# Optimization experiments

Hardware: AMD Instinct MI355X
Metric: run time of the kernel (lower is better)

The kernel has to match this reference:

```python
import jax, jax.numpy as jnp
import numpy as np

EPS = 1e-5
N_HEADS = 16
D_NOPE = 128
D_ROPE = 64
D_QK = D_NOPE + D_ROPE  # 192
D_V = 128
KV_RANK = 512
SCALE = D_QK ** -0.5


def rms_norm(x, w, eps=EPS):
    return x * jax.lax.rsqrt(jnp.mean(x * x, axis=-1, keepdims=True) + eps) * w


def apply_rope(x, c, s):
    # x: [..., D_ROPE], c/s broadcastable [..., D_ROPE//2]; half-split rotation
    x0, x1 = x[..., : D_ROPE // 2], x[..., D_ROPE // 2 :]
    return jnp.concatenate([x0 * c - x1 * s, x0 * s + x1 * c], axis=-1)


def setup_inputs() -> dict:
    key = jax.random.key(0)
    ks = jax.random.split(key, 8)
    B, S, H_DIM = 2, 2048, 2048
    Q_RANK = 1536
    w = lambda k, shp: jax.random.normal(k, shp, dtype=jnp.float32) * 0.02
    # real RoPE tables: [max_seq, D_ROPE//2]
    inv_freq = 1.0 / (10000.0 ** (np.arange(0, D_ROPE, 2, dtype=np.float32) / D_ROPE))
    ang = np.arange(S, dtype=np.float32)[:, None] * inv_freq[None, :]
    return {
        "x": jax.random.normal(ks[0], (B, S, H_DIM), dtype=jnp.float32),
        "positions": jnp.arange(S, dtype=jnp.int64),
        "Wqa": w(ks[1], (H_DIM, Q_RANK)),
        "g_qa": jnp.ones((Q_RANK,), jnp.float32),
        "Wqb": w(ks[2], (Q_RANK, N_HEADS * D_QK)),
        "Wkva": w(ks[3], (H_DIM, KV_RANK + D_ROPE)),
        "g_kva": jnp.ones((KV_RANK,), jnp.float32),
        "Wkvb": w(ks[4], (KV_RANK, N_HEADS * (D_NOPE + D_V))),
        "Wo": w(ks[5], (N_HEADS * D_V, H_DIM)),
        "cos": jnp.asarray(np.cos(ang)),
        "sin": jnp.asarray(np.sin(ang)),
    }


def reference(x, positions, Wqa, g_qa, Wqb, Wkva, g_kva, Wkvb, Wo, cos, sin):
    B, S, _ = x.shape
    # Q path: low-rank down, RMSNorm, up
    q = rms_norm(x @ Wqa, g_qa) @ Wqb  # [B,S,H*D_QK]
    q = q.reshape(B, S, N_HEADS, D_QK)
    q_nope, q_rope = q[..., :D_NOPE], q[..., D_NOPE:]
    c = cos[positions]  # [S, D_ROPE//2]
    s = sin[positions]
    q_rope = apply_rope(q_rope, c[None, :, None, :], s[None, :, None, :])
    # KV path: joint down-proj, split latent / rope-key
    kv_a = x @ Wkva  # [B,S,KV_RANK+D_ROPE]
    kv_latent = rms_norm(kv_a[..., :KV_RANK], g_kva)
    k_rope = apply_rope(kv_a[..., KV_RANK:], c[None, :, :], s[None, :, :])  # [B,S,D_ROPE]
    # up-project latent to per-head k_nope and v
    kv_b = (kv_latent @ Wkvb).reshape(B, S, N_HEADS, D_NOPE + D_V)
    k_nope, v = kv_b[..., :D_NOPE], kv_b[..., D_NOPE:]
    k = jnp.concatenate(
        [k_nope, jnp.broadcast_to(k_rope[:, :, None, :], (B, S, N_HEADS, D_ROPE))], axis=-1
    )  # [B,S,H,D_QK]
    q_full = jnp.concatenate([q_nope, q_rope], axis=-1)  # [B,S,H,D_QK]
    # causal SDPA with d_qk != d_v
    scores = jnp.einsum("bqhd,bkhd->bhqk", q_full, k) * SCALE
    causal = jnp.tril(jnp.ones((S, S), dtype=bool))
    scores = jnp.where(causal[None, None, :, :], scores, -jnp.inf)
    p = jax.nn.softmax(scores, axis=-1)
    out = jnp.einsum("bhqk,bkhd->bqhd", p, v).reshape(B, S, N_HEADS * D_V)
    return out @ Wo
```

## Files before the change

kernel.cpp:

```cpp
#include <hip/hip_runtime.h>
#include <hip/hip_bf16.h>

typedef __bf16 bf16;
typedef __bf16 bf16x8 __attribute__((ext_vector_type(8)));
typedef __bf16 bf16x4 __attribute__((ext_vector_type(4)));
typedef float f32x4 __attribute__((ext_vector_type(4)));

#define B_    2
#define S_    2048
#define HD    2048
#define NH    16
#define DQK   192
#define DV    128
#define QR    1536
#define KVR   512
#define NTOK  4096
#define NKVB  4096
#define NQB   3072
#define NQKVA 2176

static __device__ __forceinline__ void gload16(const void* g, void* l) {
  __builtin_amdgcn_global_load_lds(
      (const __attribute__((address_space(1))) void*)g,
      (__attribute__((address_space(3))) void*)l, 16, 0, 0);
}

__global__ __launch_bounds__(256) void cvt_bf16(const float* __restrict__ in,
                                                bf16* __restrict__ out, long n) {
  long i = ((long)blockIdx.x * 256 + threadIdx.x) * 4;
  if (i + 3 < n) {
    float4 v = *(const float4*)(in + i);
    bf16x4 o = {(bf16)v.x, (bf16)v.y, (bf16)v.z, (bf16)v.w};
    *(bf16x4*)(out + i) = o;
  }
}

__global__ __launch_bounds__(256) void transpose_cvt(const float* __restrict__ in,
                                                     bf16* __restrict__ out,
                                                     int R, int C, int Np) {
  __shared__ float tile[32][33];
  int c0 = blockIdx.x * 32;
  int r0 = blockIdx.y * 32;
  int tx = threadIdx.x & 31, ty = threadIdx.x >> 5;
#pragma unroll
  for (int i = 0; i < 4; ++i) {
    int r = r0 + ty + i * 8, c = c0 + tx;
    tile[ty + i * 8][tx] = (c < C) ? in[(long)r * C + c] : 0.f;
  }
  __syncthreads();
#pragma unroll
  for (int i = 0; i < 4; ++i) {
    int oc = c0 + ty + i * 8;
    if (oc < Np) out[(long)oc * R + r0 + tx] = (bf16)tile[tx][ty + i * 8];
  }
}

#define GEMM_CORE(A, Bt, K)                                                    \
  __shared__ bf16 As[128 * 64];                                                \
  __shared__ bf16 Bs[128 * 64];                                                \
  const int t = threadIdx.x;                                                   \
  const int l = t & 63;                                                        \
  const int w = t >> 6;                                                        \
  const int m0 = blockIdx.y * 128;                                             \
  const int n0 = blockIdx.x * 128;                                             \
  const int wr = (w >> 1) * 64;                                                \
  const int wc = (w & 1) * 64;                                                 \
  const int lr = l & 15;                                                       \
  const int lg = l >> 4;                                                       \
  f32x4 acc[4][4] = {};                                                        \
  for (int k0 = 0; k0 < (K); k0 += 64) {                                       \
    __syncthreads();                                                           \
    _Pragma("unroll")                                                          \
    for (int j = 0; j < 4; ++j) {                                              \
      int s = j * 256 + t;                                                     \
      int row = s >> 3, sc = s & 7;                                            \
      int c = sc ^ (row & 7);                                                  \
      gload16((A) + (long)(m0 + row) * (K) + k0 + c * 8,                       \
              As + (j * 256 + w * 64) * 8);                                    \
      gload16((Bt) + (long)(n0 + row) * (K) + k0 + c * 8,                      \
              Bs + (j * 256 + w * 64) * 8);                                    \
    }                                                                          \
    __syncthreads();                                                           \
    _Pragma("unroll")                                                          \
    for (int kh = 0; kh < 2; ++kh) {                                           \
      bf16x8 af[4], bfr[4];                                                    \
      _Pragma("unroll")                                                        \
      for (int m = 0; m < 4; ++m) {                                            \
        int row = wr + m * 16 + lr;                                            \
        af[m] = *(const bf16x8*)(As + row * 64 + (((kh * 4 + lg) ^ (row & 7)) << 3)); \
      }                                                                        \
      _Pragma("unroll")                                                        \
      for (int n = 0; n < 4; ++n) {                                            \
        int row = wc + n * 16 + lr;                                            \
        bfr[n] = *(const bf16x8*)(Bs + row * 64 + (((kh * 4 + lg) ^ (row & 7)) << 3)); \
      }                                                                        \
      _Pragma("unroll")                                                        \
      for (int m = 0; m < 4; ++m)                                              \
        _Pragma("unroll")                                                      \
        for (int n = 0; n < 4; ++n)                                            \
          acc[m][n] = __builtin_amdgcn_mfma_f32_16x16x32_bf16(af[m], bfr[n], acc[m][n], 0, 0, 0); \
    }                                                                          \
  }

template <typename CT>
__global__ __launch_bounds__(256) void gemm_bf16(const bf16* __restrict__ A,
                                                 const bf16* __restrict__ Bt,
                                                 CT* __restrict__ C,
                                                 int M, int N, int K) {
  GEMM_CORE(A, Bt, K)
#pragma unroll
  for (int m = 0; m < 4; ++m)
#pragma unroll
    for (int n = 0; n < 4; ++n)
#pragma unroll
      for (int v = 0; v < 4; ++v) {
        int row = m0 + wr + m * 16 + lg * 4 + v;
        int col = n0 + wc + n * 16 + lr;
        C[(long)row * N + col] = (CT)acc[m][n][v];
      }
}

__global__ __launch_bounds__(256) void gemm_qf(const bf16* __restrict__ A,
                                               const bf16* __restrict__ Bt,
                                               const int* __restrict__ pos,
                                               const float* __restrict__ cosT,
                                               const float* __restrict__ sinT,
                                               bf16* __restrict__ q_bhsd) {
  const float SCALE = 0.07216878364870323f;
  GEMM_CORE(A, Bt, QR)
  int c0 = n0 + wc;
  int h = c0 / 192;
  int part = c0 - h * 192;
#pragma unroll
  for (int m = 0; m < 4; ++m)
#pragma unroll
    for (int v = 0; v < 4; ++v) {
      int row = m0 + wr + m * 16 + lg * 4 + v;
      int b = row >> 11, s = row & (S_ - 1);
      long base = ((long)(b * NH + h) * S_ + s) * DQK;
      if (part < 128) {
#pragma unroll
        for (int n = 0; n < 4; ++n)
          q_bhsd[base + part + n * 16 + lr] = (bf16)(acc[m][n][v] * SCALE);
      } else {
        int p = pos[s] & (S_ - 1);
        float c_lo = cosT[p * 32 + lr],      s_lo = sinT[p * 32 + lr];
        float c_hi = cosT[p * 32 + 16 + lr], s_hi = sinT[p * 32 + 16 + lr];
        float o0 = acc[m][0][v] * c_lo - acc[m][2][v] * s_lo;
        float o1 = acc[m][1][v] * c_hi - acc[m][3][v] * s_hi;
        float o2 = acc[m][0][v] * s_lo + acc[m][2][v] * c_lo;
        float o3 = acc[m][1][v] * s_hi + acc[m][3][v] * c_hi;
        q_bhsd[base + 128 + lr] = (bf16)(o0 * SCALE);
        q_bhsd[base + 144 + lr] = (bf16)(o1 * SCALE);
        q_bhsd[base + 160 + lr] = (bf16)(o2 * SCALE);
        q_bhsd[base + 176 + lr] = (bf16)(o3 * SCALE);
      }
    }
}

__global__ __launch_bounds__(256) void gemm_kvb(const bf16* __restrict__ A,
                                                const bf16* __restrict__ Bt,
                                                bf16* __restrict__ k_bhsd,
                                                bf16* __restrict__ v_rows) {
  GEMM_CORE(A, Bt, KVR)
  int c0 = n0 + wc;
  int h = c0 >> 8;
  int dbase = c0 & 64;
  bool vpart = (c0 >> 7) & 1;
#pragma unroll
  for (int m = 0; m < 4; ++m)
#pragma unroll
    for (int v = 0; v < 4; ++v) {
      int row = m0 + wr + m * 16 + lg * 4 + v;
      int b = row >> 11, s = row & (S_ - 1);
      if (!vpart) {
        long base = ((long)(b * NH + h) * S_ + s) * DQK + dbase;
#pragma unroll
        for (int n = 0; n < 4; ++n)
          k_bhsd[base + n * 16 + lr] = (bf16)acc[m][n][v];
      } else {
        long base = (long)row * 2048 + h * 128 + dbase;
#pragma unroll
        for (int n = 0; n < 4; ++n)
          v_rows[base + n * 16 + lr] = (bf16)acc[m][n][v];
      }
    }
}

__global__ __launch_bounds__(192) void rmsnorm_q(const bf16* __restrict__ in,
                                                 const float* __restrict__ g,
                                                 bf16* __restrict__ out) {
  int row = blockIdx.x;
  int t = threadIdx.x;
  const bf16* x = in + (long)row * NQKVA;
  bf16x8 vv = *(const bf16x8*)(x + t * 8);
  float vf[8]; float ss = 0.f;
#pragma unroll
  for (int e = 0; e < 8; ++e) { vf[e] = (float)vv[e]; ss += vf[e] * vf[e]; }
#pragma unroll
  for (int m = 1; m < 64; m <<= 1) ss += __shfl_xor(ss, m);
  __shared__ float red[3];
  if ((t & 63) == 0) red[t >> 6] = ss;
  __syncthreads();
  ss = red[0] + red[1] + red[2];
  float rs = rsqrtf(ss / QR + 1e-5f);
  bf16x8 o;
#pragma unroll
  for (int e = 0; e < 8; ++e) o[e] = (bf16)(vf[e] * rs * g[t * 8 + e]);
  *(bf16x8*)(out + (long)row * QR + t * 8) = o;
}

__global__ __launch_bounds__(64) void kv_prep(const bf16* __restrict__ xa,
                                              const float* __restrict__ g,
                                              const int* __restrict__ pos,
                                              const float* __restrict__ cosT,
                                              const float* __restrict__ sinT,
                                              bf16* __restrict__ kv_l,
                                              bf16* __restrict__ k_bhsd) {
  int row = blockIdx.x;
  int t = threadIdx.x;
  int b = row >> 11, s = row & (S_ - 1);
  const bf16* x = xa + (long)row * NQKVA + QR;
  bf16x8 vv = *(const bf16x8*)(x + t * 8);
  float vf[8]; float ss = 0.f;
#pragma unroll
  for (int e = 0; e < 8; ++e) { vf[e] = (float)vv[e]; ss += vf[e] * vf[e]; }
#pragma unroll
  for (int m = 1; m < 64; m <<= 1) ss += __shfl_xor(ss, m);
  float rs = rsqrtf(ss / KVR + 1e-5f);
  bf16x8 o;
#pragma unroll
  for (int e = 0; e < 8; ++e) o[e] = (bf16)(vf[e] * rs * g[t * 8 + e]);
  *(bf16x8*)(kv_l + (long)row * KVR + t * 8) = o;
  __shared__ bf16 rope_s[64];
  if (t < 32) {
    int p = pos[s] & (S_ - 1);
    float c = cosT[p * 32 + t], sn = sinT[p * 32 + t];
    float x0 = (float)x[512 + t], x1 = (float)x[544 + t];
    rope_s[t] = (bf16)(x0 * c - x1 * sn);
    rope_s[32 + t] = (bf16)(x0 * sn + x1 * c);
  }
  __syncthreads();
  bf16x8 rv = *(const bf16x8*)&rope_s[(t & 7) * 8];
  long base0 = ((long)(b * NH + (t >> 3)) * S_ + s) * DQK + 128 + (t & 7) * 8;
  long base1 = ((long)(b * NH + 8 + (t >> 3)) * S_ + s) * DQK + 128 + (t & 7) * 8;
  *(bf16x8*)(k_bhsd + base0) = rv;
  *(bf16x8*)(k_bhsd + base1) = rv;
}

__global__ __launch_bounds__(256) void v_trans(const bf16* __restrict__ v_rows,
                                               bf16* __restrict__ v_t) {
  __shared__ bf16 tile[32][33];
  int st = blockIdx.x, dt = blockIdx.y, bh = blockIdx.z;
  int b = bh >> 4, h = bh & 15;
  int tx = threadIdx.x & 31, ty = threadIdx.x >> 5;
#pragma unroll
  for (int i = 0; i < 4; ++i) {
    int s = st * 32 + ty + i * 8, d = dt * 32 + tx;
    tile[ty + i * 8][tx] = v_rows[((long)(b * S_ + s)) * 2048 + h * 128 + d];
  }
  __syncthreads();
#pragma unroll
  for (int i = 0; i < 4; ++i) {
    int d = dt * 32 + ty + i * 8, s = st * 32 + tx;
    v_t[((long)bh * DV + d) * S_ + s] = tile[tx][ty + i * 8];
  }
}

#define QBLK 64
#define KVB  64
__global__ __launch_bounds__(256) void flash2(const bf16* __restrict__ q_bhsd,
                                              const bf16* __restrict__ k_bhsd,
                                              const bf16* __restrict__ v_t,
                                              bf16* __restrict__ att) {
  __shared__ bf16 Ks[KVB * DQK];
  __shared__ bf16 Vs[DV * KVB];
  __shared__ bf16 Ps[4][16 * 72];
  int bid = blockIdx.x;
  int bh = bid & 31;
  int qt = 31 - (bid >> 5);
  int b = bh >> 4, h = bh & 15;
  int q0 = qt * QBLK;
  int t = threadIdx.x;
  int w = t >> 6, l = t & 63;
  int lr = l & 15, lg = l >> 4;
  int qw = q0 + w * 16;

  const bf16* Qb = q_bhsd + (long)bh * S_ * DQK;
  const bf16* Kb = k_bhsd + (long)bh * S_ * DQK;
  const bf16* Vb = v_t + (long)bh * DV * S_;

  bf16x8 qf[6];
#pragma unroll
  for (int t6 = 0; t6 < 6; ++t6)
    qf[t6] = *(const bf16x8*)(Qb + (long)(qw + lr) * DQK + t6 * 32 + lg * 8);

  f32x4 oacc[8] = {};
  float mrow[4] = {-1e30f, -1e30f, -1e30f, -1e30f};
  float lrow[4] = {0.f, 0.f, 0.f, 0.f};
  const int lr7 = lr & 7;

  int nkt = qt + 1;
  for (int kt = 0; kt < nkt; ++kt) {
    int k0 = kt * KVB;
    __syncthreads();
#pragma unroll
    for (int j = 0; j < 6; ++j) {
      int s = j * 256 + t;
      int r = s / 24, c1 = s - r * 24;
      int c = c1 ^ (r & 7);
      gload16(Kb + (long)(k0 + r) * DQK + c * 8, Ks + (j * 256 + w * 64) * 8);
    }
#pragma unroll
    for (int j = 0; j < 4; ++j) {
      int s = j * 256 + t;
      int d = s >> 3, c1 = s & 7;
      int c = c1 ^ (d & 7);
      gload16(Vb + (long)d * S_ + k0 + c * 8, Vs + (j * 256 + w * 64) * 8);
    }
    __syncthreads();
    if (k0 > qw + 15) continue;

    f32x4 sacc[4] = {};
#pragma unroll
    for (int n = 0; n < 4; ++n) {
      int rk = n * 16 + lr;
#pragma unroll
      for (int t6 = 0; t6 < 6; ++t6) {
        bf16x8 kf = *(const bf16x8*)(Ks + rk * DQK + (((t6 * 4 + lg) ^ lr7) << 3));
        sacc[n] = __builtin_amdgcn_mfma_f32_16x16x32_bf16(qf[t6], kf, sacc[n], 0, 0, 0);
      }
    }
    if (k0 + KVB - 1 > qw) {
#pragma unroll
      for (int n = 0; n < 4; ++n)
#pragma unroll
        for (int v = 0; v < 4; ++v) {
          int r = lg * 4 + v, c = n * 16 + lr;
          if (k0 + c > qw + r) sacc[n][v] = -1e30f;
        }
    }
    float corr[4], p[4][4];
#pragma unroll
    for (int v = 0; v < 4; ++v) {
      float mv = fmaxf(fmaxf(sacc[0][v], sacc[1][v]), fmaxf(sacc[2][v], sacc[3][v]));
#pragma unroll
      for (int msk = 1; msk < 16; msk <<= 1) mv = fmaxf(mv, __shfl_xor(mv, msk));
      float mt = fmaxf(mrow[v], mv);
      corr[v] = __expf(mrow[v] - mt);
      float ps = 0.f;
#pragma unroll
      for (int n = 0; n < 4; ++n) { p[n][v] = __expf(sacc[n][v] - mt); ps += p[n][v]; }
#pragma unroll
      for (int msk = 1; msk < 16; msk <<= 1) ps += __shfl_xor(ps, msk);
      lrow[v] = lrow[v] * corr[v] + ps;
      mrow[v] = mt;
    }
#pragma unroll
    for (int dn = 0; dn < 8; ++dn)
#pragma unroll
      for (int v = 0; v < 4; ++v) oacc[dn][v] *= corr[v];
#pragma unroll
    for (int v = 0; v < 4; ++v)
#pragma unroll
      for (int n = 0; n < 4; ++n)
        Ps[w][(lg * 4 + v) * 72 + n * 16 + lr] = (bf16)p[n][v];
#pragma unroll
    for (int kc = 0; kc < 2; ++kc) {
      bf16x8 pf = *(const bf16x8*)(Ps[w] + lr * 72 + kc * 32 + lg * 8);
#pragma unroll
      for (int dn = 0; dn < 8; ++dn) {
        int d = dn * 16 + lr;
        bf16x8 vf = *(const bf16x8*)(Vs + d * KVB + (((kc * 4 + lg) ^ lr7) << 3));
        oacc[dn] = __builtin_amdgcn_mfma_f32_16x16x32_bf16(pf, vf, oacc[dn], 0, 0, 0);
      }
    }
  }
#pragma unroll
  for (int dn = 0; dn < 8; ++dn)
#pragma unroll
    for (int v = 0; v < 4; ++v) {
      int r = lg * 4 + v;
      float o = oacc[dn][v] / lrow[v];
      att[((long)(b * S_ + qw + r)) * 2048 + h * 128 + dn * 16 + lr] = (bf16)o;
    }
}

extern "C" void kernel_launch(void* const* d_in, const int* in_sizes, int n_in,
                              void* d_out, int out_size, void* d_ws, size_t ws_size,
                              hipStream_t stream) {
  const float* x        = (const float*)d_in[0];
  const int* pos        = (const int*)d_in[1];
  const float* Wqa      = (const float*)d_in[2];
  const float* g_qa     = (const float*)d_in[3];
  const float* Wqb      = (const float*)d_in[4];
  const float* Wkva     = (const float*)d_in[5];
  const float* g_kva    = (const float*)d_in[6];
  const float* Wkvb     = (const float*)d_in[7];
  const float* Wo       = (const float*)d_in[8];
  const float* cosT     = (const float*)d_in[9];
  const float* sinT     = (const float*)d_in[10];
  float* out            = (float*)d_out;

  size_t off = 0;
  char* wsp = (char*)d_ws;
  auto alloc = [&](size_t n) { void* p = wsp + off; off += (n + 255) & ~(size_t)255; return p; };
  bf16*  Wqa_t  = (bf16*) alloc((size_t)QR * HD * 2);
  bf16*  Wkva_t = (bf16*) alloc((size_t)640 * HD * 2);
  bf16*  Wqb_t  = (bf16*) alloc((size_t)NQB * QR * 2);
  bf16*  Wkvb_t = (bf16*) alloc((size_t)NKVB * KVR * 2);
  bf16*  Wo_t   = (bf16*) alloc((size_t)HD * HD * 2);
  bf16*  x_bf   = (bf16*) alloc((size_t)NTOK * HD * 2);
  bf16*  q_bhsd = (bf16*) alloc((size_t)B_ * NH * S_ * DQK * 2);
  bf16*  k_bhsd = (bf16*) alloc((size_t)B_ * NH * S_ * DQK * 2);
  bf16*  v_rows = (bf16*) alloc((size_t)NTOK * 2048 * 2);
  bf16*  v_t    = (bf16*) alloc((size_t)B_ * NH * DV * S_ * 2);
  bf16*  att    = (bf16*) alloc((size_t)NTOK * 2048 * 2);
  char*  T      = (char*) alloc((size_t)33554432);
  bf16*  xa  = (bf16*)T;
  bf16*  q_n = (bf16*)(T + 18874368);
  bf16*  kv_l = (bf16*)(T + 18874368);
  if (ws_size < off) return;

  cvt_bf16<<<(NTOK * HD / 4 + 255) / 256, 256, 0, stream>>>(x, x_bf, (long)NTOK * HD);
  transpose_cvt<<<dim3(QR / 32, HD / 32), 256, 0, stream>>>(Wqa, Wqa_t, HD, QR, QR);
  transpose_cvt<<<dim3(640 / 32, HD / 32), 256, 0, stream>>>(Wkva, Wkva_t, HD, 576, 640);
  transpose_cvt<<<dim3(NQB / 32, QR / 32), 256, 0, stream>>>(Wqb, Wqb_t, QR, NQB, NQB);
  transpose_cvt<<<dim3(NKVB / 32, KVR / 32), 256, 0, stream>>>(Wkvb, Wkvb_t, KVR, NKVB, NKVB);
  transpose_cvt<<<dim3(HD / 32, HD / 32), 256, 0, stream>>>(Wo, Wo_t, HD, HD, HD);
  gemm_bf16<bf16><<<dim3(NQKVA / 128, NTOK / 128), 256, 0, stream>>>(x_bf, Wqa_t, xa, NTOK, NQKVA, HD);
  rmsnorm_q<<<NTOK, 192, 0, stream>>>(xa, g_qa, q_n);
  gemm_qf<<<dim3(NQB / 128, NTOK / 128), 256, 0, stream>>>(q_n, Wqb_t, pos, cosT, sinT, q_bhsd);
  kv_prep<<<NTOK, 64, 0, stream>>>(xa, g_kva, pos, cosT, sinT, kv_l, k_bhsd);
  gemm_kvb<<<dim3(NKVB / 128, NTOK / 128), 256, 0, stream>>>(kv_l, Wkvb_t, k_bhsd, v_rows);
  v_trans<<<dim3(S_ / 32, DV / 32, B_ * NH), 256, 0, stream>>>(v_rows, v_t);
  flash2<<<1024, 256, 0, stream>>>(q_bhsd, k_bhsd, v_t, att);
  gemm_bf16<float><<<dim3(HD / 128, NTOK / 128), 256, 0, stream>>>(att, Wo_t, out, NTOK, HD, HD);
}
```

Baseline: 357.8 us.

## Fuse Q/KV norm kernels, use exp2 softmax, compute row sums via MFMA ones column

Merges the Q RMSNorm and KV norm+RoPE kernels into one launch, giving kv_l its own workspace region so both outputs can be live at once. The Q scale now folds in log2(e) so flash attention can use the hardware exp2 instruction instead of __expf. The softmax row-sum shuffle reduction is dropped: an extra V row of ones is appended in LDS so the row sum comes out of one additional MFMA column. This trades a 9th MFMA per chunk and some extra LDS for fewer shuffles and exponent ops.

Result: faster. 334.8 us (-6.4%).

```diff
diff --git a/kernel.cpp b/kernel.cpp
--- a/kernel.cpp
+++ b/kernel.cpp
@@ -18,6 +18,8 @@
 #define NKVB  4096
 #define NQB   3072
 #define NQKVA 2176
+
+#define EXP2F(x) __builtin_amdgcn_exp2f(x)
 
 static __device__ __forceinline__ void gload16(const void* g, void* l) {
   __builtin_amdgcn_global_load_lds(
@@ -126,7 +128,7 @@
                                                const float* __restrict__ cosT,
                                                const float* __restrict__ sinT,
                                                bf16* __restrict__ q_bhsd) {
-  const float SCALE = 0.07216878364870323f;
+  const float SCALE = 0.07216878364870323f * 1.4426950408889634f;
   GEMM_CORE(A, Bt, QR)
   int c0 = n0 + wc;
   int h = c0 / 192;
@@ -187,65 +189,68 @@
     }
 }
 
-__global__ __launch_bounds__(192) void rmsnorm_q(const bf16* __restrict__ in,
-                                                 const float* __restrict__ g,
-                                                 bf16* __restrict__ out) {
-  int row = blockIdx.x;
-  int t = threadIdx.x;
-  const bf16* x = in + (long)row * NQKVA;
-  bf16x8 vv = *(const bf16x8*)(x + t * 8);
-  float vf[8]; float ss = 0.f;
-#pragma unroll
-  for (int e = 0; e < 8; ++e) { vf[e] = (float)vv[e]; ss += vf[e] * vf[e]; }
-#pragma unroll
-  for (int m = 1; m < 64; m <<= 1) ss += __shfl_xor(ss, m);
-  __shared__ float red[3];
-  if ((t & 63) == 0) red[t >> 6] = ss;
-  __syncthreads();
-  ss = red[0] + red[1] + red[2];
-  float rs = rsqrtf(ss / QR + 1e-5f);
-  bf16x8 o;
-#pragma unroll
-  for (int e = 0; e < 8; ++e) o[e] = (bf16)(vf[e] * rs * g[t * 8 + e]);
-  *(bf16x8*)(out + (long)row * QR + t * 8) = o;
-}
-
-__global__ __launch_bounds__(64) void kv_prep(const bf16* __restrict__ xa,
-                                              const float* __restrict__ g,
-                                              const int* __restrict__ pos,
-                                              const float* __restrict__ cosT,
-                                              const float* __restrict__ sinT,
-                                              bf16* __restrict__ kv_l,
-                                              bf16* __restrict__ k_bhsd) {
+__global__ __launch_bounds__(256) void norm_prep(const bf16* __restrict__ xa,
+                                                 const float* __restrict__ g_qa,
+                                                 const float* __restrict__ g_kva,
+                                                 const int* __restrict__ pos,
+                                                 const float* __restrict__ cosT,
+                                                 const float* __restrict__ sinT,
+                                                 bf16* __restrict__ q_n,
+                                                 bf16* __restrict__ kv_l,
+                                                 bf16* __restrict__ k_bhsd) {
   int row = blockIdx.x;
   int t = threadIdx.x;
   int b = row >> 11, s = row & (S_ - 1);
-  const bf16* x = xa + (long)row * NQKVA + QR;
-  bf16x8 vv = *(const bf16x8*)(x + t * 8);
-  float vf[8]; float ss = 0.f;
-#pragma unroll
-  for (int e = 0; e < 8; ++e) { vf[e] = (float)vv[e]; ss += vf[e] * vf[e]; }
-#pragma unroll
-  for (int m = 1; m < 64; m <<= 1) ss += __shfl_xor(ss, m);
-  float rs = rsqrtf(ss / KVR + 1e-5f);
-  bf16x8 o;
-#pragma unroll
-  for (int e = 0; e < 8; ++e) o[e] = (bf16)(vf[e] * rs * g[t * 8 + e]);
-  *(bf16x8*)(kv_l + (long)row * KVR + t * 8) = o;
+  const bf16* xr = xa + (long)row * NQKVA;
+  __shared__ float red[3];
   __shared__ bf16 rope_s[64];
-  if (t < 32) {
-    int p = pos[s] & (S_ - 1);
-    float c = cosT[p * 32 + t], sn = sinT[p * 32 + t];
-    float x0 = (float)x[512 + t], x1 = (float)x[544 + t];
-    rope_s[t] = (bf16)(x0 * c - x1 * sn);
-    rope_s[32 + t] = (bf16)(x0 * sn + x1 * c);
+  float vf[8];
+  if (t < 192) {
+    bf16x8 vv = *(const bf16x8*)(xr + t * 8);
+    float ss = 0.f;
+#pragma unroll
+    for (int e = 0; e < 8; ++e) { vf[e] = (float)vv[e]; ss += vf[e] * vf[e]; }
+#pragma unroll
+    for (int m = 1; m < 64; m <<= 1) ss += __shfl_xor(ss, m);
+    if ((t & 63) == 0) red[t >> 6] = ss;
+  } else {
+    int tt = t - 192;
+    const bf16* xl = xr + QR;
+    bf16x8 vv = *(const bf16x8*)(xl + tt * 8);
+    float ss = 0.f;
+#pragma unroll
+    for (int e = 0; e < 8; ++e) { vf[e] = (float)vv[e]; ss += vf[e] * vf[e]; }
+#pragma unroll
+    for (int m = 1; m < 64; m <<= 1) ss += __shfl_xor(ss, m);
+    float rs = rsqrtf(ss / KVR + 1e-5f);
+    bf16x8 o;
+#pragma unroll
+    for (int e = 0; e < 8; ++e) o[e] = (bf16)(vf[e] * rs * g_kva[tt * 8 + e]);
+    *(bf16x8*)(kv_l + (long)row * KVR + tt * 8) = o;
+    if (tt < 32) {
+      int p = pos[s] & (S_ - 1);
+      float c = cosT[p * 32 + tt], sn = sinT[p * 32 + tt];
+      float x0 = (float)xl[512 + tt], x1 = (float)xl[544 + tt];
+      rope_s[tt] = (bf16)(x0 * c - x1 * sn);
+      rope_s[32 + tt] = (bf16)(x0 * sn + x1 * c);
+    }
   }
   __syncthreads();
-  bf16x8 rv = *(const bf16x8*)&rope_s[(t & 7) * 8];
-  long base0 = ((long)(b * NH + (t >> 3)) * S_ + s) * DQK + 128 + (t & 7) * 8;
-  long base1 = ((long)(b * NH + 8 + (t >> 3)) * S_ + s) * DQK + 128 + (t & 7) * 8;
-  *(bf16x8*)(k_bhsd + base0) = rv;
-  *(bf16x8*)(k_bhsd + base1) = rv;
+  if (t < 192) {
+    float ss = red[0] + red[1] + red[2];
+    float rs = rsqrtf(ss / QR + 1e-5f);
+    bf16x8 o;
+#pragma unroll
+    for (int e = 0; e < 8; ++e) o[e] = (bf16)(vf[e] * rs * g_qa[t * 8 + e]);
+    *(bf16x8*)(q_n + (long)row * QR + t * 8) = o;
+  } else {
+    int tt = t - 192;
+    bf16x8 rv = *(const bf16x8*)&rope_s[(tt & 7) * 8];
+    long base0 = ((long)(b * NH + (tt >> 3)) * S_ + s) * DQK + 128 + (tt & 7) * 8;
+    long base1 = ((long)(b * NH + 8 + (tt >> 3)) * S_ + s) * DQK + 128 + (tt & 7) * 8;
+    *(bf16x8*)(k_bhsd + base0) = rv;
+    *(bf16x8*)(k_bhsd + base1) = rv;
+  }
 }
 
 __global__ __launch_bounds__(256) void v_trans(const bf16* __restrict__ v_rows,
@@ -269,12 +274,13 @@
 
 #define QBLK 64
 #define KVB  64
+#define DVP  144
 __global__ __launch_bounds__(256) void flash2(const bf16* __restrict__ q_bhsd,
                                               const bf16* __restrict__ k_bhsd,
                                               const bf16* __restrict__ v_t,
                                               bf16* __restrict__ att) {
   __shared__ bf16 Ks[KVB * DQK];
-  __shared__ bf16 Vs[DV * KVB];
+  __shared__ bf16 Vs[DVP * KVB];
   __shared__ bf16 Ps[4][16 * 72];
   int bid = blockIdx.x;
   int bh = bid & 31;
@@ -290,14 +296,20 @@
   const bf16* Kb = k_bhsd + (long)bh * S_ * DQK;
   const bf16* Vb = v_t + (long)bh * DV * S_;
 
+  if (t < 128) {
+    int rr = 128 + (t >> 3), cc = (t & 7) * 8;
+    bf16 val = (bf16)((rr == 128) ? 1.0f : 0.0f);
+    bf16x8 vvv = {val, val, val, val, val, val, val, val};
+    *(bf16x8*)(Vs + rr * KVB + cc) = vvv;
+  }
+
   bf16x8 qf[6];
 #pragma unroll
   for (int t6 = 0; t6 < 6; ++t6)
     qf[t6] = *(const bf16x8*)(Qb + (long)(qw + lr) * DQK + t6 * 32 + lg * 8);
 
-  f32x4 oacc[8] = {};
+  f32x4 oacc[9] = {};
   float mrow[4] = {-1e30f, -1e30f, -1e30f, -1e30f};
-  float lrow[4] = {0.f, 0.f, 0.f, 0.f};
   const int lr7 = lr & 7;
 
   int nkt = qt + 1;
@@ -347,17 +359,13 @@
 #pragma unroll
       for (int msk = 1; msk < 16; msk <<= 1) mv = fmaxf(mv, __shfl_xor(mv, msk));
       float mt = fmaxf(mrow[v], mv);
-      corr[v] = __expf(mrow[v] - mt);
-      float ps = 0.f;
-#pragma unroll
-      for (int n = 0; n < 4; ++n) { p[n][v] = __expf(sacc[n][v] - mt); ps += p[n][v]; }
-#pragma unroll
-      for (int msk = 1; msk < 16; msk <<= 1) ps += __shfl_xor(ps, msk);
-      lrow[v] = lrow[v] * corr[v] + ps;
+      corr[v] = EXP2F(mrow[v] - mt);
+#pragma unroll
+      for (int n = 0; n < 4; ++n) p[n][v] = EXP2F(sacc[n][v] - mt);
       mrow[v] = mt;
     }
 #pragma unroll
-    for (int dn = 0; dn < 8; ++dn)
+    for (int dn = 0; dn < 9; ++dn)
 #pragma unroll
       for (int v = 0; v < 4; ++v) oacc[dn][v] *= corr[v];
 #pragma unroll
@@ -369,19 +377,25 @@
     for (int kc = 0; kc < 2; ++kc) {
       bf16x8 pf = *(const bf16x8*)(Ps[w] + lr * 72 + kc * 32 + lg * 8);
 #pragma unroll
-      for (int dn = 0; dn < 8; ++dn) {
+      for (int dn = 0; dn < 9; ++dn) {
         int d = dn * 16 + lr;
         bf16x8 vf = *(const bf16x8*)(Vs + d * KVB + (((kc * 4 + lg) ^ lr7) << 3));
         oacc[dn] = __builtin_amdgcn_mfma_f32_16x16x32_bf16(pf, vf, oacc[dn], 0, 0, 0);
       }
     }
   }
+  float rl[4];
+#pragma unroll
+  for (int v = 0; v < 4; ++v) {
+    float lv = __shfl(oacc[8][v], lg * 16);
+    rl[v] = 1.0f / lv;
+  }
 #pragma unroll
   for (int dn = 0; dn < 8; ++dn)
 #pragma unroll
     for (int v = 0; v < 4; ++v) {
       int r = lg * 4 + v;
-      float o = oacc[dn][v] / lrow[v];
+      float o = oacc[dn][v] * rl[v];
       att[((long)(b * S_ + qw + r)) * 2048 + h * 128 + dn * 16 + lr] = (bf16)o;
     }
 }
@@ -419,7 +433,7 @@
   char*  T      = (char*) alloc((size_t)33554432);
   bf16*  xa  = (bf16*)T;
   bf16*  q_n = (bf16*)(T + 18874368);
-  bf16*  kv_l = (bf16*)(T + 18874368);
+  bf16*  kv_l = (bf16*)(T + 18874368 + 12582912);
   if (ws_size < off) return;
 
   cvt_bf16<<<(NTOK * HD / 4 + 255) / 256, 256, 0, stream>>>(x, x_bf, (long)NTOK * HD);
@@ -429,9 +443,8 @@
   transpose_cvt<<<dim3(NKVB / 32, KVR / 32), 256, 0, stream>>>(Wkvb, Wkvb_t, KVR, NKVB, NKVB);
   transpose_cvt<<<dim3(HD / 32, HD / 32), 256, 0, stream>>>(Wo, Wo_t, HD, HD, HD);
   gemm_bf16<bf16><<<dim3(NQKVA / 128, NTOK / 128), 256, 0, stream>>>(x_bf, Wqa_t, xa, NTOK, NQKVA, HD);
-  rmsnorm_q<<<NTOK, 192, 0, stream>>>(xa, g_qa, q_n);
+  norm_prep<<<NTOK, 256, 0, stream>>>(xa, g_qa, g_kva, pos, cosT, sinT, q_n, kv_l, k_bhsd);
   gemm_qf<<<dim3(NQB / 128, NTOK / 128), 256, 0, stream>>>(q_n, Wqb_t, pos, cosT, sinT, q_bhsd);
-  kv_prep<<<NTOK, 64, 0, stream>>>(xa, g_kva, pos, cosT, sinT, kv_l, k_bhsd);
   gemm_kvb<<<dim3(NKVB / 128, NTOK / 128), 256, 0, stream>>>(kv_l, Wkvb_t, k_bhsd, v_rows);
   v_trans<<<dim3(S_ / 32, DV / 32, B_ * NH), 256, 0, stream>>>(v_rows, v_t);
   flash2<<<1024, 256, 0, stream>>>(q_bhsd, k_bhsd, v_t, att);
```
